# Kernel optimization log

Measured on AMD Instinct MI355X. Metric: run time of the kernel, lower is better.

## Reference

```python
import jax, jax.numpy as jnp
import numpy as np
from jax import lax

B, H, W, C = 2, 256, 256, 192
HEADS = 6
WS = 8                      # window size
PW = WS // 2                # permuted window size (kv downsampled 2x2)
HIDDEN = 4 * C
HEAD_DIM = C // HEADS
SCALE = HEAD_DIM ** -0.5
N_WIN = WS * WS             # 64 query tokens per window
N_KV = PW * PW              # 16 kv tokens per window


def _aligned_index(pw0, pw1):
    ch = np.arange(pw0)
    cw = np.arange(pw1)
    coords = np.stack(np.meshgrid(ch, cw, indexing='ij'))          # (2, pw0, pw1)
    cf = coords.reshape(2, -1)
    rel = (cf[:, :, None] - cf[:, None, :]).transpose(1, 2, 0).astype(np.int64)
    rel[:, :, 0] += pw0 - 1
    rel[:, :, 1] += pw1 - 1
    rel[:, :, 0] *= 2 * pw1 - 1
    idx = rel.sum(-1)                                              # (N_KV, N_KV)
    n4 = pw0 * pw1
    idx = idx.reshape(pw0, pw1, 1, 1, n4)
    idx = np.tile(idx, (1, 1, 2, 2, 1)).transpose(0, 2, 1, 3, 4).reshape(4 * n4, n4)
    return jnp.asarray(idx)

IDX = _aligned_index(PW, PW)   # (N_WIN, N_KV)


def layernorm(x, g, b):
    mu = x.mean(-1, keepdims=True)
    var = ((x - mu) ** 2).mean(-1, keepdims=True)
    return (x - mu) * lax.rsqrt(var + 1e-5) * g + b


def window_partition(x):
    # (B, H, W, C) -> (B*nW, WS, WS, C)
    x = x.reshape(B, H // WS, WS, W // WS, WS, C)
    return x.transpose(0, 1, 3, 2, 4, 5).reshape(-1, WS, WS, C)


def window_reverse(w):
    # (B*nW, WS, WS, C) -> (B, H, W, C)
    x = w.reshape(B, H // WS, W // WS, WS, WS, C)
    return x.transpose(0, 1, 3, 2, 4, 5).reshape(B, H, W, C)


def setup_inputs() -> dict:
    key = jax.random.key(0)
    ks = jax.random.split(key, 10)
    rn = lambda k, shp, s=0.02: jax.random.normal(k, shp, jnp.float32) * s
    return {
        'x': jax.random.normal(ks[0], (B, H * W, C), jnp.float32),
        'g1': jnp.ones((C,), jnp.float32), 'be1': jnp.zeros((C,), jnp.float32),
        'wq': rn(ks[1], (C, C)), 'bq': jnp.zeros((C,), jnp.float32),
        'wkv': rn(ks[2], (C, C // 2)), 'bkv': jnp.zeros((C // 2,), jnp.float32),
        'bias_table': rn(ks[3], ((2 * PW - 1) * (2 * PW - 1), HEADS)),
        'wproj': rn(ks[4], (C, C)), 'bproj': jnp.zeros((C,), jnp.float32),
        'g2': jnp.ones((C,), jnp.float32), 'be2': jnp.zeros((C,), jnp.float32),
        'w1f': rn(ks[5], (C, HIDDEN)), 'b1f': jnp.zeros((HIDDEN,), jnp.float32),
        'dwk': rn(ks[6], (HIDDEN, 1, 5, 5)), 'dwb': jnp.zeros((HIDDEN,), jnp.float32),
        'w2f': rn(ks[7], (HIDDEN, C)), 'b2f': jnp.zeros((C,), jnp.float32),
    }


def reference(x, g1, be1, wq, bq, wkv, bkv, bias_table, wproj, bproj,
              g2, be2, w1f, b1f, dwk, dwb, w2f, b2f):
    shortcut = x
    xn = layernorm(x, g1, be1).reshape(B, H, W, C)
    xw = window_partition(xn).reshape(-1, N_WIN, C)        # (b_, 64, C)
    b_ = xw.shape[0]
    # PSA: kv downsampled 2x2 spatially, 2x2 block folded into channels
    kv = (xw @ wkv + bkv).reshape(b_, PW, 2, PW, 2, 2, C // 4)
    kv = kv.transpose(0, 1, 3, 5, 2, 4, 6).reshape(b_, N_KV, 2, HEADS, HEAD_DIM)
    kv = kv.transpose(2, 0, 3, 1, 4)                       # (2, b_, h, N_KV, d)
    k, v = kv[0], kv[1]
    q = (xw @ wq + bq).reshape(b_, N_WIN, HEADS, HEAD_DIM).transpose(0, 2, 1, 3) * SCALE
    attn = jnp.einsum('bhqd,bhkd->bhqk', q, k)             # (b_, h, 64, 16)
    bias = bias_table[IDX.reshape(-1)].reshape(N_WIN, N_KV, HEADS).transpose(2, 0, 1)
    attn = jax.nn.softmax(attn + bias[None], axis=-1)
    aw = jnp.einsum('bhqk,bhkd->bhqd', attn, v).transpose(0, 2, 1, 3).reshape(b_, N_WIN, C)
    aw = aw @ wproj + bproj
    x = shortcut + window_reverse(aw.reshape(-1, WS, WS, C)).reshape(B, H * W, C)
    # ConvFFN with depthwise-conv residual branch
    xn2 = layernorm(x, g2, be2)
    h1 = jax.nn.gelu(xn2 @ w1f + b1f, approximate=False)   # (B, HW, HIDDEN)
    img = h1.transpose(0, 2, 1).reshape(B, HIDDEN, H, W)
    conv = lax.conv_general_dilated(img, dwk, (1, 1), ((2, 2), (2, 2)),
                                    feature_group_count=HIDDEN,
                                    dimension_numbers=('NCHW', 'OIHW', 'NCHW'))
    conv = jax.nn.gelu(conv + dwb[None, :, None, None], approximate=False)
    h = h1 + conv.reshape(B, HIDDEN, H * W).transpose(0, 2, 1)
    return x + (h @ w2f + b2f)
```

## Files before the change

### kernel.cpp

```cpp
#include <hip/hip_runtime.h>
#include <hip/hip_bf16.h>
#include <math.h>

#define NTOK  131072
#define NTOKH 65536
#define CD    192
#define HID   768

typedef short bf16x8 __attribute__((ext_vector_type(8)));
typedef float f32x4  __attribute__((ext_vector_type(4)));
typedef float f32x2  __attribute__((ext_vector_type(2)));

__device__ __forceinline__ float bf2f(unsigned short v) {
    union { unsigned int u; float f; } c; c.u = ((unsigned int)v) << 16; return c.f;
}
__device__ __forceinline__ unsigned short f2bf(float f) {
    union { float f; unsigned int u; } c; c.f = f;
    unsigned int r = c.u + 0x7FFFu + ((c.u >> 16) & 1u);
    return (unsigned short)(r >> 16);
}
__device__ __forceinline__ float gelu_f(float x) {
    float t = x * 0.7071067811865476f;
    t = fminf(fmaxf(t, -4.0f), 4.0f);
    float s2 = t * t;
    float p = fmaf(s2, -2.72614225801306e-10f, 2.77068142495902e-08f);
    p = fmaf(s2, p, -2.10102402082508e-06f);
    p = fmaf(s2, p, -5.69250639462346e-05f);
    p = fmaf(s2, p, -7.34990630326855e-04f);
    p = fmaf(s2, p, -2.95459980854025e-03f);
    p = fmaf(s2, p, -1.60960333262415e-02f);
    p = p * t;
    float q = fmaf(s2, -1.45660718464996e-05f, -2.13374055278905e-04f);
    q = fmaf(s2, q, -1.68282697438203e-03f);
    q = fmaf(s2, q, -7.37332916720468e-03f);
    q = fmaf(s2, q, -1.42647390514189e-02f);
    float er = p * __builtin_amdgcn_rcpf(q);
    return 0.5f * x * (1.0f + er);
}

__device__ __forceinline__ void gld16(const unsigned short* g, unsigned short* l) {
    __builtin_amdgcn_global_load_lds(
        (const __attribute__((address_space(1))) void*)(unsigned long long)(g),
        (__attribute__((address_space(3))) void*)(unsigned int)(unsigned long long)(l),
        16, 0, 0);
}

__global__ __launch_bounds__(256) void ln_kernel(const float* __restrict__ x,
                                                 const float* __restrict__ g,
                                                 const float* __restrict__ b,
                                                 unsigned short* __restrict__ out) {
    int tok  = blockIdx.x * 4 + (threadIdx.x >> 6);
    int lane = threadIdx.x & 63;
    const float* xp = x + (size_t)tok * CD;
    float v0 = xp[lane], v1 = xp[lane + 64], v2 = xp[lane + 128];
    float s  = v0 + v1 + v2;
    float s2 = v0 * v0 + v1 * v1 + v2 * v2;
    #pragma unroll
    for (int off = 32; off > 0; off >>= 1) {
        s  += __shfl_xor(s,  off, 64);
        s2 += __shfl_xor(s2, off, 64);
    }
    float mu  = s * (1.0f / 192.0f);
    float var = s2 * (1.0f / 192.0f) - mu * mu;
    float rs  = rsqrtf(var + 1e-5f);
    unsigned short* op = out + (size_t)tok * CD;
    op[lane]       = f2bf((v0 - mu) * rs * g[lane]       + b[lane]);
    op[lane + 64]  = f2bf((v1 - mu) * rs * g[lane + 64]  + b[lane + 64]);
    op[lane + 128] = f2bf((v2 - mu) * rs * g[lane + 128] + b[lane + 128]);
}

__global__ __launch_bounds__(256) void wconv_kernel(
    const float* __restrict__ wq, const float* __restrict__ wkv,
    const float* __restrict__ wproj, const float* __restrict__ w1f,
    const float* __restrict__ w2f,
    unsigned short* __restrict__ qkvT, unsigned short* __restrict__ projT,
    unsigned short* __restrict__ w1T, unsigned short* __restrict__ w2T)
{
    int i = blockIdx.x * 256 + threadIdx.x;
    if (i < 288 * 192) {
        int n = i / 192, k = i - n * 192;
        float v = (n < 192) ? wq[(size_t)k * 192 + n] : wkv[(size_t)k * 96 + (n - 192)];
        qkvT[n * 192 + k] = f2bf(v);
    }
    if (i < 192 * 192) {
        int n = i / 192, k = i - n * 192;
        projT[n * 192 + k] = f2bf(wproj[(size_t)k * 192 + n]);
    }
    {
        int n = i / 192, k = i - n * 192;
        w1T[n * 192 + k] = f2bf(w1f[(size_t)k * 768 + n]);
    }
    {
        int n = i / 768, k = i - n * 768;
        w2T[n * 768 + k] = f2bf(w2f[(size_t)k * 192 + n]);
    }
}

__device__ __forceinline__ void xcd_swz(int gx, int& bx, int& by) {
    int nwg  = gx * (int)gridDim.y;
    int id   = (int)blockIdx.y * gx + (int)blockIdx.x;
    int q    = nwg >> 3, r = nwg & 7;
    int xcd  = id & 7, rest = id >> 3;
    int sw   = (xcd < r ? xcd * (q + 1) : r * (q + 1) + (xcd - r) * q) + rest;
    bx = sw % gx; by = sw / gx;
}

template<int MODE>
__global__ __launch_bounds__(256) void mgemm_kernel(
    const unsigned short* __restrict__ A,
    const unsigned short* __restrict__ WT,
    const float* __restrict__ b0, const float* __restrict__ b1,
    const float* __restrict__ addsrc,
    void* O0, unsigned short* __restrict__ O1,
    int K, int Nreal)
{
    constexpr int BM = 128, BN = 96, BK = 64;
    __shared__ unsigned short As[BM * BK];
    __shared__ unsigned short Bs[BN * BK];
    const int tid  = threadIdx.x;
    const int wave = tid >> 6, lane = tid & 63;
    const int quad = lane >> 4, l16 = lane & 15;
    const int wm = (wave >> 1) * 64, wn = (wave & 1) * 48;
    int bx, by; xcd_swz(gridDim.x, bx, by);
    const int m0 = by * BM, n0 = bx * BN;

    f32x4 acc[4][3];
    #pragma unroll
    for (int mi = 0; mi < 4; mi++)
        #pragma unroll
        for (int ni = 0; ni < 3; ni++) acc[mi][ni] = (f32x4){0.f, 0.f, 0.f, 0.f};

    const int r8 = lane >> 3;
    const int sw = ((lane & 7) ^ r8) << 3;
    const unsigned short* aSrc = A  + (size_t)(m0 + wave * 32 + r8) * K + sw;
    const unsigned short* bSrc = WT + (size_t)(n0 + wave * 24 + r8) * K + sw;
    unsigned short* aDst = &As[(wave * 32) * BK];
    unsigned short* bDst = &Bs[(wave * 24) * BK];

    for (int k0 = 0; k0 < K; k0 += BK) {
        #pragma unroll
        for (int i = 0; i < 4; i++)
            gld16(aSrc + k0 + i * 8 * K, aDst + i * 8 * BK);
        #pragma unroll
        for (int i = 0; i < 3; i++)
            gld16(bSrc + k0 + i * 8 * K, bDst + i * 8 * BK);
        __syncthreads();

        #pragma unroll
        for (int kk = 0; kk < 2; kk++) {
            const int cb = kk * 64 + quad * 16;
            bf16x8 bfr[3];
            #pragma unroll
            for (int ni = 0; ni < 3; ni++) {
                int br = wn + ni * 16 + l16;
                bfr[ni] = *(const bf16x8*)&Bs[br * BK + ((cb ^ ((br & 7) << 4)) >> 1)];
            }
            #pragma unroll
            for (int mi = 0; mi < 4; mi++) {
                int ar = wm + mi * 16 + l16;
                bf16x8 af = *(const bf16x8*)&As[ar * BK + ((cb ^ ((ar & 7) << 4)) >> 1)];
                acc[mi][0] = __builtin_amdgcn_mfma_f32_16x16x32_bf16(af, bfr[0], acc[mi][0], 0, 0, 0);
                acc[mi][1] = __builtin_amdgcn_mfma_f32_16x16x32_bf16(af, bfr[1], acc[mi][1], 0, 0, 0);
                acc[mi][2] = __builtin_amdgcn_mfma_f32_16x16x32_bf16(af, bfr[2], acc[mi][2], 0, 0, 0);
            }
        }
        __syncthreads();
    }

    float bc[3], bc1[3];
    #pragma unroll
    for (int ni = 0; ni < 3; ni++) {
        int col = n0 + wn + ni * 16 + l16;
        if (MODE == 0) {
            if (n0 < 192) bc[ni] = b0[col];
            else          bc1[ni] = b1[col - 192];
        } else {
            bc[ni] = b0[col];
        }
    }
    #pragma unroll
    for (int mi = 0; mi < 4; mi++) {
        int row0 = m0 + wm + mi * 16 + quad * 4;
        #pragma unroll
        for (int r = 0; r < 4; r++) {
            unsigned mrow = (unsigned)(row0 + r);
            if (MODE == 0) {
                if (n0 < 192) {
                    unsigned ob = mrow * 192u + (unsigned)(n0 + wn + l16);
                    unsigned short* q0 = (unsigned short*)O0;
                    #pragma unroll
                    for (int ni = 0; ni < 3; ni++)
                        q0[ob + ni * 16] = f2bf((acc[mi][ni][r] + bc[ni]) * 0.17677669529663687f);
                } else {
                    unsigned ob = mrow * 96u + (unsigned)(n0 - 192 + wn + l16);
                    #pragma unroll
                    for (int ni = 0; ni < 3; ni++)
                        O1[ob + ni * 16] = f2bf(acc[mi][ni][r] + bc1[ni]);
                }
            } else if (MODE == 1) {
                unsigned ob = mrow * 192u + (unsigned)(n0 + wn + l16);
                float* op = (float*)O0;
                #pragma unroll
                for (int ni = 0; ni < 3; ni++)
                    op[ob + ni * 16] = acc[mi][ni][r] + bc[ni] + addsrc[ob + ni * 16];
            } else if (MODE == 2) {
                unsigned ob = mrow * 768u + (unsigned)(n0 + wn + l16);
                unsigned short* op = (unsigned short*)O0;
                #pragma unroll
                for (int ni = 0; ni < 3; ni++)
                    op[ob + ni * 16] = f2bf(gelu_f(acc[mi][ni][r] + bc[ni]));
            } else {
                unsigned ob = mrow * 192u + (unsigned)(n0 + wn + l16);
                float* op = (float*)O0;
                #pragma unroll
                for (int ni = 0; ni < 3; ni++)
                    op[ob + ni * 16] = op[ob + ni * 16] + acc[mi][ni][r] + bc[ni];
            }
        }
    }
}

__global__ __launch_bounds__(384) void attn_kernel(
    const unsigned short* __restrict__ q, const unsigned short* __restrict__ kvp,
    const float* __restrict__ bt, unsigned short* __restrict__ aw)
{
    __shared__ float ks[6][16][32];
    __shared__ float vs[6][16][32];
    const int w = blockIdx.x;
    const int b = w >> 10, rem = w & 1023, wh = rem >> 5, wc = rem & 31;
    const int tid = threadIdx.x;
    const size_t base = (size_t)b * 65536;

    for (int e = tid; e < 16 * 192; e += 384) {
        int kk = e / 192, f = e - kk * 192;
        int d1 = kk >> 2, d3 = kk & 3;
        int d2 = f / 96;  int r = f - d2 * 96;
        int d4 = r / 48;  int c4 = r - d4 * 48;
        int i = 2 * d1 + d2, j = 2 * d3 + d4;
        size_t g = base + (size_t)(wh * 8 + i) * 256 + (wc * 8 + j);
        int h = f >> 5, d = f & 31;
        ks[h][kk][d] = bf2f(kvp[g * 96 + c4]);
        vs[h][kk][d] = bf2f(kvp[g * 96 + 48 + c4]);
    }
    __syncthreads();

    const int t = tid & 63, h = tid >> 6;
    const int i = t >> 3, j = t & 7;
    const int iq2 = i >> 1, jq2 = j >> 1;
    const size_t g = base + (size_t)(wh * 8 + i) * 256 + (wc * 8 + j);

    f32x2 qr[16];
    const ushort4* qp = (const ushort4*)(q + g * 192 + h * 32);
    #pragma unroll
    for (int d4i = 0; d4i < 8; d4i++) {
        ushort4 u = qp[d4i];
        qr[d4i * 2 + 0] = (f32x2){bf2f(u.x), bf2f(u.y)};
        qr[d4i * 2 + 1] = (f32x2){bf2f(u.z), bf2f(u.w)};
    }

    float lg[16]; float mx = -1e30f;
    #pragma unroll
    for (int kk = 0; kk < 16; kk++) {
        int kh = kk >> 2, kw = kk & 3;
        const f32x2* kp = (const f32x2*)&ks[h][kk][0];
        f32x2 a2 = (f32x2){bt[((iq2 - kh + 3) * 7 + (jq2 - kw + 3)) * 6 + h], 0.f};
        #pragma unroll
        for (int d = 0; d < 16; d++) a2 = __builtin_elementwise_fma(qr[d], kp[d], a2);
        float s = a2.x + a2.y;
        lg[kk] = s; mx = fmaxf(mx, s);
    }
    float den = 0.f;
    #pragma unroll
    for (int kk = 0; kk < 16; kk++) { lg[kk] = expf(lg[kk] - mx); den += lg[kk]; }
    float inv = 1.0f / den;

    f32x2 oacc[16];
    #pragma unroll
    for (int d = 0; d < 16; d++) oacc[d] = (f32x2){0.f, 0.f};
    #pragma unroll
    for (int kk = 0; kk < 16; kk++) {
        float p = lg[kk] * inv;
        f32x2 pv = (f32x2){p, p};
        const f32x2* vp = (const f32x2*)&vs[h][kk][0];
        #pragma unroll
        for (int d = 0; d < 16; d++) oacc[d] = __builtin_elementwise_fma(pv, vp[d], oacc[d]);
    }
    unsigned int* op = (unsigned int*)(aw + g * 192 + h * 32);
    #pragma unroll
    for (int d = 0; d < 16; d++) {
        unsigned int lo = f2bf(oacc[d].x), hi = f2bf(oacc[d].y);
        op[d] = lo | (hi << 16);
    }
}

__global__ __launch_bounds__(256) void dwconv_kernel(
    const unsigned short* __restrict__ h1,
    const float* __restrict__ dwk, const float* __restrict__ dwb,
    unsigned short* __restrict__ hout)
{
    __shared__ unsigned short tile[12][12][64];
    int bx = blockIdx.x;
    int chb = bx % 12; int t = bx / 12;
    int tw = t % 32; int th = t / 32;
    const int tid = threadIdx.x;
    const int chbase = chb * 64;
    const int ch = tid & 63;
    const int cp = tid >> 6;
    const int c0 = cp * 2;

    float w[25];
    #pragma unroll
    for (int tap = 0; tap < 25; tap++)
        w[tap] = dwk[(size_t)(chbase + ch) * 25 + tap];
    const float bias = dwb[chbase + ch];

    const int lane4 = tid & 15;
    const int pg = tid >> 4;
    for (int p = pg; p < 144; p += 16) {
        int pr = p / 12, pc = p - pr * 12;
        int r = th * 8 - 2 + pr, c = tw * 8 - 2 + pc;
        ushort4 u = make_ushort4(0, 0, 0, 0);
        if (r >= 0 && r < 256 && c >= 0 && c < 256)
            u = *(const ushort4*)(h1 + (((size_t)r * 256 + c) * HID + chbase + lane4 * 4));
        *(ushort4*)&tile[pr][pc][lane4 * 4] = u;
    }
    __syncthreads();

    float win[5][6];
    #pragma unroll
    for (int rr = 0; rr < 4; rr++)
        #pragma unroll
        for (int cc = 0; cc < 6; cc++)
            win[rr][cc] = bf2f(tile[rr][c0 + cc][ch]);

    unsigned obase = ((unsigned)(th * 8) * 256u + (unsigned)(tw * 8 + c0)) * (unsigned)HID
                   + (unsigned)(chbase + ch);

    #pragma unroll
    for (int r0 = 0; r0 < 8; r0++) {
        #pragma unroll
        for (int cc = 0; cc < 6; cc++)
            win[(r0 + 4) % 5][cc] = bf2f(tile[r0 + 4][c0 + cc][ch]);
        float s0 = bias, s1 = bias;
        #pragma unroll
        for (int kr = 0; kr < 5; kr++) {
            int ri = (r0 + kr) % 5;
            #pragma unroll
            for (int kc = 0; kc < 5; kc++) {
                float wt = w[kr * 5 + kc];
                s0 = fmaf(win[ri][kc],     wt, s0);
                s1 = fmaf(win[ri][kc + 1], wt, s1);
            }
        }
        const int rc = (r0 + 2) % 5;
        float v0 = win[rc][2] + gelu_f(s0);
        float v1 = win[rc][3] + gelu_f(s1);
        hout[obase]       = f2bf(v0);
        hout[obase + HID] = f2bf(v1);
        obase += 256u * (unsigned)HID;
    }
}

extern "C" void kernel_launch(void* const* d_in, const int* in_sizes, int n_in,
                              void* d_out, int out_size, void* d_ws, size_t ws_size,
                              hipStream_t stream) {
    const float* x    = (const float*)d_in[0];
    const float* g1   = (const float*)d_in[1];
    const float* be1  = (const float*)d_in[2];
    const float* wq   = (const float*)d_in[3];
    const float* bq   = (const float*)d_in[4];
    const float* wkv  = (const float*)d_in[5];
    const float* bkv  = (const float*)d_in[6];
    const float* btab = (const float*)d_in[7];
    const float* wproj= (const float*)d_in[8];
    const float* bproj= (const float*)d_in[9];
    const float* g2   = (const float*)d_in[10];
    const float* be2  = (const float*)d_in[11];
    const float* w1f  = (const float*)d_in[12];
    const float* b1f  = (const float*)d_in[13];
    const float* dwk  = (const float*)d_in[14];
    const float* dwb  = (const float*)d_in[15];
    const float* w2f  = (const float*)d_in[16];
    const float* b2f  = (const float*)d_in[17];
    float* out = (float*)d_out;

    char* ws = (char*)d_ws;
    unsigned short* xnb  = (unsigned short*)(ws);
    unsigned short* qb   = (unsigned short*)(ws + 50331648);
    unsigned short* kvb  = (unsigned short*)(ws + 100663296);
    unsigned short* h1b  = (unsigned short*)(ws + 125829120);
    unsigned short* hhb  = (unsigned short*)(ws + 226492416);
    unsigned short* qkvT = (unsigned short*)(ws + 327155712);
    unsigned short* projT= (unsigned short*)(ws + 327266304);
    unsigned short* w1T  = (unsigned short*)(ws + 327340032);
    unsigned short* w2T  = (unsigned short*)(ws + 327634944);

    wconv_kernel<<<576, 256, 0, stream>>>(wq, wkv, wproj, w1f, w2f,
                                          qkvT, projT, w1T, w2T);
    ln_kernel<<<NTOK / 4, 256, 0, stream>>>(x, g1, be1, xnb);
    mgemm_kernel<0><<<dim3(3, NTOK / 128), 256, 0, stream>>>(
        xnb, qkvT, bq, bkv, nullptr, qb, kvb, 192, 288);
    attn_kernel<<<2048, 384, 0, stream>>>(qb, kvb, btab, xnb);
    mgemm_kernel<1><<<dim3(2, NTOK / 128), 256, 0, stream>>>(
        xnb, projT, bproj, nullptr, x, out, nullptr, 192, 192);
    ln_kernel<<<NTOK / 4, 256, 0, stream>>>(out, g2, be2, qb);
    for (int half = 0; half < 2; half++) {
        const unsigned short* xn2h = qb + (size_t)half * NTOKH * CD;
        float* outh = out + (size_t)half * NTOKH * CD;
        mgemm_kernel<2><<<dim3(8, NTOKH / 128), 256, 0, stream>>>(
            xn2h, w1T, b1f, nullptr, nullptr, h1b, nullptr, 192, 768);
        dwconv_kernel<<<12 * 32 * 32, 256, 0, stream>>>(h1b, dwk, dwb, hhb);
        mgemm_kernel<3><<<dim3(2, NTOKH / 128), 256, 0, stream>>>(
            hhb, w2T, b2f, nullptr, nullptr, outh, nullptr, 768, 192);
    }
}
```

Before: 728.6 us.

## Fuse projection GEMM with residual add and LayerNorm; pack dwconv math into float2

Replaces the projection GEMM plus separate LayerNorm pass with one kernel. Each block computes a full 192-column output row tile, adds bias and the residual, writes the fp32 result, then reduces row statistics across waves through shared memory and writes the normalized bf16 activations. This drops one full read of the fp32 intermediate and one kernel launch, at the cost of wider accumulator tiles and more registers per block. The depthwise conv also computes its two output columns as packed float2 FMAs and a vectorized GELU, aiming at packed-FMA instructions.

```diff
diff --git a/kernel.cpp b/kernel.cpp
--- a/kernel.cpp
+++ b/kernel.cpp
@@ -36,6 +36,28 @@
     q = fmaf(s2, q, -1.42647390514189e-02f);
     float er = p * __builtin_amdgcn_rcpf(q);
     return 0.5f * x * (1.0f + er);
+}
+__device__ __forceinline__ f32x2 gelu2(f32x2 x) {
+    f32x2 t = x * (f32x2){0.7071067811865476f, 0.7071067811865476f};
+    t = __builtin_elementwise_min(
+            __builtin_elementwise_max(t, (f32x2){-4.f, -4.f}), (f32x2){4.f, 4.f});
+    f32x2 s2 = t * t;
+    f32x2 p = __builtin_elementwise_fma(s2, (f32x2){-2.72614225801306e-10f, -2.72614225801306e-10f},
+                                        (f32x2){2.77068142495902e-08f, 2.77068142495902e-08f});
+    p = __builtin_elementwise_fma(s2, p, (f32x2){-2.10102402082508e-06f, -2.10102402082508e-06f});
+    p = __builtin_elementwise_fma(s2, p, (f32x2){-5.69250639462346e-05f, -5.69250639462346e-05f});
+    p = __builtin_elementwise_fma(s2, p, (f32x2){-7.34990630326855e-04f, -7.34990630326855e-04f});
+    p = __builtin_elementwise_fma(s2, p, (f32x2){-2.95459980854025e-03f, -2.95459980854025e-03f});
+    p = __builtin_elementwise_fma(s2, p, (f32x2){-1.60960333262415e-02f, -1.60960333262415e-02f});
+    p = p * t;
+    f32x2 q = __builtin_elementwise_fma(s2, (f32x2){-1.45660718464996e-05f, -1.45660718464996e-05f},
+                                        (f32x2){-2.13374055278905e-04f, -2.13374055278905e-04f});
+    q = __builtin_elementwise_fma(s2, q, (f32x2){-1.68282697438203e-03f, -1.68282697438203e-03f});
+    q = __builtin_elementwise_fma(s2, q, (f32x2){-7.37332916720468e-03f, -7.37332916720468e-03f});
+    q = __builtin_elementwise_fma(s2, q, (f32x2){-1.42647390514189e-02f, -1.42647390514189e-02f});
+    f32x2 er = {p.x * __builtin_amdgcn_rcpf(q.x), p.y * __builtin_amdgcn_rcpf(q.y)};
+    f32x2 one = {1.f, 1.f};
+    return (f32x2){0.5f, 0.5f} * x * (one + er);
 }
 
 __device__ __forceinline__ void gld16(const unsigned short* g, unsigned short* l) {
@@ -197,12 +219,6 @@
                     for (int ni = 0; ni < 3; ni++)
                         O1[ob + ni * 16] = f2bf(acc[mi][ni][r] + bc1[ni]);
                 }
-            } else if (MODE == 1) {
-                unsigned ob = mrow * 192u + (unsigned)(n0 + wn + l16);
-                float* op = (float*)O0;
-                #pragma unroll
-                for (int ni = 0; ni < 3; ni++)
-                    op[ob + ni * 16] = acc[mi][ni][r] + bc[ni] + addsrc[ob + ni * 16];
             } else if (MODE == 2) {
                 unsigned ob = mrow * 768u + (unsigned)(n0 + wn + l16);
                 unsigned short* op = (unsigned short*)O0;
@@ -216,6 +232,126 @@
                 for (int ni = 0; ni < 3; ni++)
                     op[ob + ni * 16] = op[ob + ni * 16] + acc[mi][ni][r] + bc[ni];
             }
+        }
+    }
+}
+
+__global__ __launch_bounds__(256) void projln_kernel(
+    const unsigned short* __restrict__ A,
+    const unsigned short* __restrict__ WT,
+    const float* __restrict__ bpj,
+    const float* __restrict__ xres,
+    const float* __restrict__ g2, const float* __restrict__ be2,
+    float* __restrict__ out, unsigned short* __restrict__ xn2)
+{
+    constexpr int BM = 128, BN = 192, BK = 64, K = 192;
+    __shared__ unsigned short As[BM * BK];
+    __shared__ unsigned short Bs[BN * BK];
+    const int tid  = threadIdx.x;
+    const int wave = tid >> 6, lane = tid & 63;
+    const int quad = lane >> 4, l16 = lane & 15;
+    const int wm = (wave >> 1) * 64, wn = (wave & 1) * 96;
+    int id = blockIdx.x;
+    int swz = (id & 7) * 128 + (id >> 3);
+    const int m0 = swz * BM;
+
+    f32x4 acc[4][6];
+    #pragma unroll
+    for (int mi = 0; mi < 4; mi++)
+        #pragma unroll
+        for (int ni = 0; ni < 6; ni++) acc[mi][ni] = (f32x4){0.f, 0.f, 0.f, 0.f};
+
+    const int r8 = lane >> 3;
+    const int sw = ((lane & 7) ^ r8) << 3;
+    const unsigned short* aSrc = A  + (size_t)(m0 + wave * 32 + r8) * K + sw;
+    const unsigned short* bSrc = WT + (size_t)(wave * 48 + r8) * K + sw;
+    unsigned short* aDst = &As[(wave * 32) * BK];
+    unsigned short* bDst = &Bs[(wave * 48) * BK];
+
+    for (int k0 = 0; k0 < K; k0 += BK) {
+        #pragma unroll
+        for (int i = 0; i < 4; i++)
+            gld16(aSrc + k0 + i * 8 * K, aDst + i * 8 * BK);
+        #pragma unroll
+        for (int i = 0; i < 6; i++)
+            gld16(bSrc + k0 + i * 8 * K, bDst + i * 8 * BK);
+        __syncthreads();
+
+        #pragma unroll
+        for (int kk = 0; kk < 2; kk++) {
+            const int cb = kk * 64 + quad * 16;
+            bf16x8 bfr[6];
+            #pragma unroll
+            for (int ni = 0; ni < 6; ni++) {
+                int br = wn + ni * 16 + l16;
+                bfr[ni] = *(const bf16x8*)&Bs[br * BK + ((cb ^ ((br & 7) << 4)) >> 1)];
+            }
+            #pragma unroll
+            for (int mi = 0; mi < 4; mi++) {
+                int ar = wm + mi * 16 + l16;
+                bf16x8 af = *(const bf16x8*)&As[ar * BK + ((cb ^ ((ar & 7) << 4)) >> 1)];
+                #pragma unroll
+                for (int ni = 0; ni < 6; ni++)
+                    acc[mi][ni] = __builtin_amdgcn_mfma_f32_16x16x32_bf16(af, bfr[ni], acc[mi][ni], 0, 0, 0);
+            }
+        }
+        __syncthreads();
+    }
+
+    float bc[6], g2c[6], be2c[6];
+    #pragma unroll
+    for (int ni = 0; ni < 6; ni++) {
+        int col = wn + ni * 16 + l16;
+        bc[ni] = bpj[col]; g2c[ni] = g2[col]; be2c[ni] = be2[col];
+    }
+    float* red = (float*)As;
+    #pragma unroll
+    for (int mi = 0; mi < 4; mi++) {
+        float s1[4] = {0.f, 0.f, 0.f, 0.f}, s2[4] = {0.f, 0.f, 0.f, 0.f};
+        #pragma unroll
+        for (int r = 0; r < 4; r++) {
+            unsigned mrow = (unsigned)(m0 + wm + mi * 16 + quad * 4 + r);
+            unsigned ob = mrow * 192u + (unsigned)(wn + l16);
+            #pragma unroll
+            for (int ni = 0; ni < 6; ni++) {
+                float y = acc[mi][ni][r] + bc[ni] + xres[ob + ni * 16];
+                out[ob + ni * 16] = y;
+                acc[mi][ni][r] = y;
+                s1[r] += y; s2[r] += y * y;
+            }
+        }
+        #pragma unroll
+        for (int off = 1; off < 16; off <<= 1) {
+            #pragma unroll
+            for (int r = 0; r < 4; r++) {
+                s1[r] += __shfl_xor(s1[r], off, 64);
+                s2[r] += __shfl_xor(s2[r], off, 64);
+            }
+        }
+        if (l16 == 0) {
+            #pragma unroll
+            for (int r = 0; r < 4; r++) {
+                int row = wm + mi * 16 + quad * 4 + r;
+                red[row * 4 + (wave & 1) * 2 + 0] = s1[r];
+                red[row * 4 + (wave & 1) * 2 + 1] = s2[r];
+            }
+        }
+    }
+    __syncthreads();
+    #pragma unroll
+    for (int mi = 0; mi < 4; mi++) {
+        #pragma unroll
+        for (int r = 0; r < 4; r++) {
+            int row = wm + mi * 16 + quad * 4 + r;
+            float S1 = red[row * 4 + 0] + red[row * 4 + 2];
+            float S2 = red[row * 4 + 1] + red[row * 4 + 3];
+            float mu  = S1 * (1.0f / 192.0f);
+            float var = S2 * (1.0f / 192.0f) - mu * mu;
+            float rs  = rsqrtf(var + 1e-5f);
+            unsigned ob = (unsigned)(m0 + row) * 192u + (unsigned)(wn + l16);
+            #pragma unroll
+            for (int ni = 0; ni < 6; ni++)
+                xn2[ob + ni * 16] = f2bf((acc[mi][ni][r] - mu) * rs * g2c[ni] + be2c[ni]);
         }
     }
 }
@@ -326,37 +462,38 @@
     }
     __syncthreads();
 
-    float win[5][6];
+    f32x2 a[5][5];
     #pragma unroll
     for (int rr = 0; rr < 4; rr++)
         #pragma unroll
-        for (int cc = 0; cc < 6; cc++)
-            win[rr][cc] = bf2f(tile[rr][c0 + cc][ch]);
+        for (int kc = 0; kc < 5; kc++)
+            a[rr][kc] = (f32x2){bf2f(tile[rr][c0 + kc][ch]), bf2f(tile[rr][c0 + kc + 1][ch])};
 
     unsigned obase = ((unsigned)(th * 8) * 256u + (unsigned)(tw * 8 + c0)) * (unsigned)HID
                    + (unsigned)(chbase + ch);
 
     #pragma unroll
     for (int r0 = 0; r0 < 8; r0++) {
-        #pragma unroll
-        for (int cc = 0; cc < 6; cc++)
-            win[(r0 + 4) % 5][cc] = bf2f(tile[r0 + 4][c0 + cc][ch]);
-        float s0 = bias, s1 = bias;
+        const int rn = (r0 + 4) % 5;
+        #pragma unroll
+        for (int kc = 0; kc < 5; kc++)
+            a[rn][kc] = (f32x2){bf2f(tile[r0 + 4][c0 + kc][ch]),
+                                bf2f(tile[r0 + 4][c0 + kc + 1][ch])};
+
+        f32x2 s = (f32x2){bias, bias};
         #pragma unroll
         for (int kr = 0; kr < 5; kr++) {
-            int ri = (r0 + kr) % 5;
+            const int ri = (r0 + kr) % 5;
             #pragma unroll
             for (int kc = 0; kc < 5; kc++) {
                 float wt = w[kr * 5 + kc];
-                s0 = fmaf(win[ri][kc],     wt, s0);
-                s1 = fmaf(win[ri][kc + 1], wt, s1);
+                s = __builtin_elementwise_fma((f32x2){wt, wt}, a[ri][kc], s);
             }
         }
         const int rc = (r0 + 2) % 5;
-        float v0 = win[rc][2] + gelu_f(s0);
-        float v1 = win[rc][3] + gelu_f(s1);
-        hout[obase]       = f2bf(v0);
-        hout[obase + HID] = f2bf(v1);
+        f32x2 v = a[rc][2] + gelu2(s);
+        hout[obase]       = f2bf(v.x);
+        hout[obase + HID] = f2bf(v.y);
         obase += 256u * (unsigned)HID;
     }
 }
@@ -401,9 +538,8 @@
     mgemm_kernel<0><<<dim3(3, NTOK / 128), 256, 0, stream>>>(
         xnb, qkvT, bq, bkv, nullptr, qb, kvb, 192, 288);
     attn_kernel<<<2048, 384, 0, stream>>>(qb, kvb, btab, xnb);
-    mgemm_kernel<1><<<dim3(2, NTOK / 128), 256, 0, stream>>>(
-        xnb, projT, bproj, nullptr, x, out, nullptr, 192, 192);
-    ln_kernel<<<NTOK / 4, 256, 0, stream>>>(out, g2, be2, qb);
+    projln_kernel<<<1024, 256, 0, stream>>>(
+        xnb, projT, bproj, x, g2, be2, out, qb);
     for (int half = 0; half < 2; half++) {
         const unsigned short* xn2h = qb + (size_t)half * NTOKH * CD;
         float* outh = out + (size_t)half * NTOKH * CD;
```

After: 814.6 us. +11.8%, slower.
